# Performance work log

Hardware: AMD Instinct MI355X
Metric: run time of the kernel (lower is better)

Reference implementation:

```python
import jax, jax.numpy as jnp
import numpy as np

EPS = 1e-5

def conv1x1(x, w):
    # x: (B,C,H,W), w: (O,C) -> (B,O,H,W)
    return jnp.einsum('bchw,oc->bohw', x, w)

def bn_relu(y, g, b, m, v):
    s = g / jnp.sqrt(v + EPS)
    return jax.nn.relu(y * s[None, :, None, None] + (b - m * s)[None, :, None, None])

def cbr(x, w, g, b, m, v):
    return bn_relu(conv1x1(x, w), g, b, m, v)

def _bn_params(key, c):
    k1, k2, k3, k4 = jax.random.split(key, 4)
    g = 1.0 + 0.1 * jax.random.normal(k1, (c,), jnp.float32)
    b = 0.1 * jax.random.normal(k2, (c,), jnp.float32)
    m = 0.05 * jax.random.normal(k3, (c,), jnp.float32)
    v = jax.random.uniform(k4, (c,), jnp.float32, 0.5, 1.5)
    return g, b, m, v

def setup_inputs() -> dict:
    key = jax.random.key(0)
    B, Cin, H, W = 8, 512, 64, 64
    Ck, Cv, Cout = 256, 256, 512
    ks = jax.random.split(key, 12)
    def w(k, o, c):
        return jax.random.normal(k, (o, c), jnp.float32) * (1.0 / np.sqrt(c))
    inp = {}
    inp['x'] = jax.random.normal(ks[0], (B, Cin, H, W), jnp.float32)
    # f_key
    inp['kW1'] = w(ks[1], Ck, Cin); inp['kG1'], inp['kB1'], inp['kM1'], inp['kV1'] = _bn_params(ks[2], Ck)
    inp['kW2'] = w(ks[3], Ck, Ck);  inp['kG2'], inp['kB2'], inp['kM2'], inp['kV2'] = _bn_params(ks[4], Ck)
    # f_query
    inp['qW1'] = w(ks[5], Ck, Cin); inp['qG1'], inp['qB1'], inp['qM1'], inp['qV1'] = _bn_params(ks[6], Ck)
    inp['qW2'] = w(ks[7], Ck, Ck);  inp['qG2'], inp['qB2'], inp['qM2'], inp['qV2'] = _bn_params(ks[8], Ck)
    # f_value
    inp['vW'] = w(ks[9], Cv, Cin)
    # W (output projection)
    inp['wW'] = w(ks[10], Cout, Cv); inp['wG'], inp['wB'], inp['wM'], inp['wV'] = _bn_params(ks[11], Cout)
    return inp

def reference(x,
              kW1, kG1, kB1, kM1, kV1, kW2, kG2, kB2, kM2, kV2,
              qW1, qG1, qB1, qM1, qV1, qW2, qG2, qB2, qM2, qV2,
              vW,
              wW, wG, wB, wM, wV):
    B, _, H, W = x.shape
    q = cbr(cbr(x, qW1, qG1, qB1, qM1, qV1), qW2, qG2, qB2, qM2, qV2)  # (B,Ck,H,W)
    k = cbr(cbr(x, kW1, kG1, kB1, kM1, kV1), kW2, kG2, kB2, kM2, kV2)  # (B,Ck,H,W)
    v = conv1x1(x, vW)                                                  # (B,Cv,H,W)
    Ck = q.shape[1]; Cv = v.shape[1]; N = H * W
    qf = q.reshape(B, Ck, N)   # query = qf^T -> (B,N,Ck)
    kf = k.reshape(B, Ck, N)
    vf = v.reshape(B, Cv, N)
    sim = jnp.einsum('bcn,bcm->bnm', qf, kf) * (Ck ** -0.5)  # (B,N,N)
    attn = jax.nn.softmax(sim, axis=-1)
    ctx = jnp.einsum('bnm,bcm->bcn', attn, vf).reshape(B, Cv, H, W)
    return cbr(ctx, wW, wG, wB, wM, wV)
```

## Files before the change

### kernel.cpp

```cpp
#include <hip/hip_runtime.h>
#include <hip/hip_bf16.h>

typedef __attribute__((ext_vector_type(8))) short bf16x8;
typedef __attribute__((ext_vector_type(4))) float f32x4;

#define MFMA16(a, b, c) __builtin_amdgcn_mfma_f32_16x16x32_bf16(a, b, c, 0, 0, 0)

static __device__ __forceinline__ unsigned short f2bf(float f) {
  union { __hip_bfloat16 h; unsigned short u; } cv;
  cv.h = __float2bfloat16(f);
  return cv.u;
}

static __device__ __forceinline__ float bf2f(short s) {
  union { float f; unsigned u; } cv;
  cv.u = ((unsigned)(unsigned short)s) << 16;
  return cv.f;
}

static __device__ __forceinline__ void gload16(const void* gptr, void* lptr) {
  __builtin_amdgcn_global_load_lds(
      (const __attribute__((address_space(1))) void*)gptr,
      (__attribute__((address_space(3))) void*)lptr, 16, 0, 0);
}


__global__ void conv_w_k(const float* __restrict__ qW1, const float* __restrict__ kW1,
                         const float* __restrict__ qW2, const float* __restrict__ kW2,
                         const float* __restrict__ vW, const float* __restrict__ wW,
                         __hip_bfloat16* __restrict__ dst) {
  int i = blockIdx.x * 256 + threadIdx.x;
  const float* src; int off;
  if (i < 131072)      { src = qW1; off = i; }
  else if (i < 262144) { src = kW1; off = i - 131072; }
  else if (i < 327680) { src = qW2; off = i - 262144; }
  else if (i < 393216) { src = kW2; off = i - 327680; }
  else if (i < 524288) { src = vW;  off = i - 393216; }
  else                 { src = wW;  off = i - 524288; }
  dst[i] = __float2bfloat16(src[off]);
}

__global__ void bn_all_k(const float* __restrict__ qG1, const float* __restrict__ qB1, const float* __restrict__ qM1, const float* __restrict__ qV1,
                         const float* __restrict__ qG2, const float* __restrict__ qB2, const float* __restrict__ qM2, const float* __restrict__ qV2,
                         const float* __restrict__ kG1, const float* __restrict__ kB1, const float* __restrict__ kM1, const float* __restrict__ kV1,
                         const float* __restrict__ kG2, const float* __restrict__ kB2, const float* __restrict__ kM2, const float* __restrict__ kV2,
                         const float* __restrict__ wG, const float* __restrict__ wB, const float* __restrict__ wM, const float* __restrict__ wV,
                         float* __restrict__ base) {
  int bidx = blockIdx.x, tid = threadIdx.x;
  const float *g, *b, *m, *v; float *s, *t; int i;
  if (bidx == 0)      { g = qG1; b = qB1; m = qM1; v = qV1; s = base;        t = base + 256;  i = tid; }
  else if (bidx == 1) { g = qG2; b = qB2; m = qM2; v = qV2; s = base + 512;  t = base + 768;  i = tid; }
  else if (bidx == 2) { g = kG1; b = kB1; m = kM1; v = kV1; s = base + 1024; t = base + 1280; i = tid; }
  else if (bidx == 3) { g = kG2; b = kB2; m = kM2; v = kV2; s = base + 1536; t = base + 1792; i = tid; }
  else                { g = wG;  b = wB;  m = wM;  v = wV;  s = base + 2048; t = base + 2560; i = (bidx - 4) * 256 + tid; }
  float sv = g[i] * rsqrtf(v[i] + 1e-5f);
  s[i] = sv;
  t[i] = b[i] - m[i] * sv;
}

__global__ __launch_bounds__(256) void transpose_k(const float* __restrict__ x,
                                                   __hip_bfloat16* __restrict__ xT) {
  __shared__ float tile[64][65];
  const int n0 = blockIdx.x * 64, c0 = blockIdx.y * 64, b = blockIdx.z;
  const int tx = threadIdx.x, ty = threadIdx.y;
  const float* xp = x + ((size_t)(b * 512 + c0) * 4096) + n0;
#pragma unroll
  for (int i = 0; i < 16; ++i) {
    int c = ty + 4 * i;
    tile[c][tx] = xp[(size_t)c * 4096 + tx];
  }
  __syncthreads();
  __hip_bfloat16* op = xT + ((size_t)(b * 4096 + n0) * 512) + c0;
#pragma unroll
  for (int i = 0; i < 16; ++i) {
    int nl = ty + 4 * i;
    op[(size_t)nl * 512 + tx] = __float2bfloat16(tile[tx][nl]);
  }
}

template <int EPI>
__global__ __launch_bounds__(256) void gemm_nt_k(
    const __hip_bfloat16* __restrict__ A, long sA,
    const __hip_bfloat16* __restrict__ B, long sB,
    void* __restrict__ Cp, long sC,
    int lda, int ldb, int ldc, int K,
    const float* __restrict__ s, const float* __restrict__ t) {
  __shared__ short As[128][72];
  __shared__ short Bs[128][72];
  const int tid = threadIdx.x;
  const int w = tid >> 6, l = tid & 63, g = l >> 4, ln = l & 15;
  const int wr = w >> 1, wc = w & 1;
  const int rb = blockIdx.x * 128, cb = blockIdx.y * 128;
  const __hip_bfloat16* Ab = A + (size_t)blockIdx.z * sA;
  const __hip_bfloat16* Bb = B + (size_t)blockIdx.z * sB;

  f32x4 acc[4][4];
#pragma unroll
  for (int i = 0; i < 4; ++i)
#pragma unroll
    for (int j = 0; j < 4; ++j) acc[i][j] = (f32x4){0.f, 0.f, 0.f, 0.f};

  const int r0 = tid >> 3;
  const int c8 = (tid & 7) * 8;

  for (int k0 = 0; k0 < K; k0 += 64) {
#pragma unroll
    for (int i = 0; i < 4; ++i) {
      const int r = r0 + 32 * i;
      *(uint4*)&As[r][c8] = *(const uint4*)(Ab + (size_t)(rb + r) * lda + (k0 + c8));
      *(uint4*)&Bs[r][c8] = *(const uint4*)(Bb + (size_t)(cb + r) * ldb + (k0 + c8));
    }
    __syncthreads();
#pragma unroll
    for (int kk = 0; kk < 2; ++kk) {
      bf16x8 av[4], bv[4];
#pragma unroll
      for (int i = 0; i < 4; ++i) av[i] = *(const bf16x8*)&As[64 * wr + 16 * i + ln][32 * kk + 8 * g];
#pragma unroll
      for (int i = 0; i < 4; ++i) bv[i] = *(const bf16x8*)&Bs[64 * wc + 16 * i + ln][32 * kk + 8 * g];
#pragma unroll
      for (int mi = 0; mi < 4; ++mi)
#pragma unroll
        for (int ni = 0; ni < 4; ++ni)
          acc[mi][ni] = MFMA16(av[mi], bv[ni], acc[mi][ni]);
    }
    __syncthreads();
  }

  const int row0 = rb + 64 * wr + 4 * g;
  const int col0 = cb + 64 * wc + ln;

  if (EPI == 2) {
    float* C = (float*)Cp + (size_t)blockIdx.z * sC;
#pragma unroll
    for (int mi = 0; mi < 4; ++mi) {
#pragma unroll
      for (int r = 0; r < 4; ++r) {
        const int R = row0 + 16 * mi + r;
        const float sr = s[R], tr = t[R];
#pragma unroll
        for (int ni = 0; ni < 4; ++ni) {
          float v = fmaf(acc[mi][ni][r], sr, tr);
          C[(size_t)R * ldc + (col0 + 16 * ni)] = v > 0.f ? v : 0.f;
        }
      }
    }
  } else {
    __hip_bfloat16* C = (__hip_bfloat16*)Cp + (size_t)blockIdx.z * sC;
    float sc[4], tc[4];
    if (EPI == 1) {
#pragma unroll
      for (int ni = 0; ni < 4; ++ni) { sc[ni] = s[col0 + 16 * ni]; tc[ni] = t[col0 + 16 * ni]; }
    }
#pragma unroll
    for (int mi = 0; mi < 4; ++mi) {
#pragma unroll
      for (int ni = 0; ni < 4; ++ni) {
#pragma unroll
        for (int r = 0; r < 4; ++r) {
          float v = acc[mi][ni][r];
          if (EPI == 1) { v = fmaf(v, sc[ni], tc[ni]); v = v > 0.f ? v : 0.f; }
          C[(size_t)(row0 + 16 * mi + r) * ldc + (col0 + 16 * ni)] = __float2bfloat16(v);
        }
      }
    }
  }
}

__global__ __launch_bounds__(256, 2) void flash_k(
    const __hip_bfloat16* __restrict__ Q,
    const __hip_bfloat16* __restrict__ Kt,
    const __hip_bfloat16* __restrict__ V,
    __hip_bfloat16* __restrict__ part,
    float* __restrict__ cArr,
    float* __restrict__ lArr) {
  __shared__ short Ks[64 * 256];
  __shared__ short Ps[64 * 64];

  const int tid = threadIdx.x;
  const int w = tid >> 6, l = tid & 63, g = l >> 4, ln = l & 15;
  const int bid = blockIdx.x;
  const int batch = bid & 7;
  const int half = (bid >> 3) & 1;
  const int qb = (bid >> 4) << 6;
  const int kvBase = half << 11;
  const size_t bo = (size_t)batch * (4096 * 256);
  const float CE = 0.09016844005556021f;

  const int swz45 = (16 * g) ^ ((ln & 3) << 4);
  const int s6 = ((ln >> 2) & 1) << 6;
  const char* Ks0 = (const char*)Ks + (ln * 512 + swz45 + s6);
  const char* Ks1 = Ks0 + (((ln >> 2) & 1) ? -64 : 64);
  const char* Pr0 = (const char*)Ps + (ln * 128 + swz45 + s6);
  const char* Pr1 = Pr0 + (((ln >> 2) & 1) ? -64 : 64);
  const int pwOff = (16 * w + ln) * 128 + 8 * (g & 1) + (((g >> 1) ^ (ln & 1)) << 4) +
                    (((ln >> 1) & 1) << 5) + s6;

  bf16x8 qf[8];
  {
    const __hip_bfloat16* qp = Q + bo + (size_t)(qb + 16 * w + ln) * 256 + 8 * g;
#pragma unroll
    for (int kk = 0; kk < 8; ++kk) qf[kk] = *(const bf16x8*)(qp + 32 * kk);
  }

  f32x4 acc[4][4];
#pragma unroll
  for (int qg = 0; qg < 4; ++qg)
#pragma unroll
    for (int ci = 0; ci < 4; ++ci) acc[qg][ci] = (f32x4){0.f, 0.f, 0.f, 0.f};
  float l_run = 0.f;
  float cval = 0.f;

  const int kRow = 16 * w + (l >> 5);
  const int kChunk = (l & 31) ^ (l >> 5);
  const short* Kb = (const short*)(Kt + bo);
  const short* Vp = (const short*)(V + bo) + (size_t)(64 * w + ln) * 4096 + 8 * g;

#define SB __builtin_amdgcn_sched_barrier(0)

#define STAGEK(M0)                                                             \
  do {                                                                         \
    _Pragma("unroll") for (int j = 0; j < 8; ++j) {                            \
      const short* gp =                                                        \
          Kb + (size_t)((M0) + kRow + 2 * j) * 256 + 8 * (kChunk ^ ((2 * j) & 7)); \
      gload16(gp, Ks + w * 4096 + j * 512);                                    \
    }                                                                          \
  } while (0)

  STAGEK(kvBase);
  SB;

  for (int t = 0; t < 32; ++t) {
    const int m0 = kvBase + (t << 6);

    bf16x8 vfr[8];
#pragma unroll
    for (int ci = 0; ci < 4; ++ci)
#pragma unroll
      for (int kk = 0; kk < 2; ++kk) {
        const short* gp = Vp + (size_t)ci * (16 * 4096) + (m0 + 32 * kk);
        asm volatile("global_load_dwordx4 %0, %1, off"
                     : "=v"(vfr[2 * ci + kk]) : "v"(gp));
      }
    SB;

    asm volatile("s_waitcnt vmcnt(8)" ::: "memory");
    SB;
    __builtin_amdgcn_s_barrier();
    asm volatile("" ::: "memory");
    SB;

    f32x4 sf[4];
#pragma unroll
    for (int mi = 0; mi < 4; ++mi) sf[mi] = (f32x4){0.f, 0.f, 0.f, 0.f};
    __builtin_amdgcn_s_setprio(1);
#pragma unroll
    for (int kk = 0; kk < 8; ++kk) {
      const char* kp = ((kk & 1) ? Ks1 : Ks0) + 128 * (kk >> 1);
#pragma unroll
      for (int mi = 0; mi < 4; ++mi) {
        bf16x8 a = *(const bf16x8*)(kp + 8192 * mi);
        sf[mi] = MFMA16(a, qf[kk], sf[mi]);
      }
    }
    __builtin_amdgcn_s_setprio(0);

    if (t == 0) {
      float a0 = fmaxf(fmaxf(sf[0][0], sf[0][1]), sf[0][2]);
      float a1 = fmaxf(fmaxf(sf[0][3], sf[1][0]), sf[1][1]);
      float a2 = fmaxf(fmaxf(sf[1][2], sf[1][3]), sf[2][0]);
      float a3 = fmaxf(fmaxf(sf[2][1], sf[2][2]), sf[2][3]);
      float a4 = fmaxf(fmaxf(sf[3][0], sf[3][1]), sf[3][2]);
      float mmax = fmaxf(fmaxf(fmaxf(fmaxf(a0, a1), a2), fmaxf(a3, a4)), sf[3][3]);
      mmax = fmaxf(mmax, __shfl_xor(mmax, 16));
      mmax = fmaxf(mmax, __shfl_xor(mmax, 32));
      cval = mmax * CE;
    }
    float psum = 0.f;
    uint2 pk[4];
#pragma unroll
    for (int mi = 0; mi < 4; ++mi) {
      float e0 = exp2f(fmaf(sf[mi][0], CE, -cval));
      float e1 = exp2f(fmaf(sf[mi][1], CE, -cval));
      float e2 = exp2f(fmaf(sf[mi][2], CE, -cval));
      float e3 = exp2f(fmaf(sf[mi][3], CE, -cval));
      psum += (e0 + e1) + (e2 + e3);
      pk[mi].x = (unsigned)f2bf(e0) | ((unsigned)f2bf(e1) << 16);
      pk[mi].y = (unsigned)f2bf(e2) | ((unsigned)f2bf(e3) << 16);
    }
    psum += __shfl_xor(psum, 16);
    psum += __shfl_xor(psum, 32);
    l_run += psum;

    {
      char* Pb = (char*)Ps;
      *(uint2*)(Pb + (pwOff ^ 0))  = pk[0];
      *(uint2*)(Pb + (pwOff ^ 32)) = pk[1];
      *(uint2*)(Pb + (pwOff ^ 64)) = pk[2];
      *(uint2*)(Pb + (pwOff ^ 96)) = pk[3];
    }

    asm volatile("s_waitcnt lgkmcnt(0)" ::: "memory");
    SB;
    __builtin_amdgcn_s_barrier();
    asm volatile("" ::: "memory");
    SB;

    if (t < 31) {
      STAGEK(m0 + 64);
      SB;
      asm volatile("s_waitcnt vmcnt(8)" ::: "memory");
    } else {
      asm volatile("s_waitcnt vmcnt(0)" ::: "memory");
    }
    SB;

    __builtin_amdgcn_s_setprio(1);
#pragma unroll
    for (int kk = 0; kk < 2; ++kk) {
#pragma unroll
      for (int qg = 0; qg < 4; ++qg) {
        bf16x8 pa = *(const bf16x8*)((kk ? Pr1 : Pr0) + 2048 * qg);
#pragma unroll
        for (int ci = 0; ci < 4; ++ci)
          acc[qg][ci] = MFMA16(pa, vfr[2 * ci + kk], acc[qg][ci]);
      }
    }
    __builtin_amdgcn_s_setprio(0);
    SB;
  }
#undef STAGEK
#undef SB

  __syncthreads();
  float* Pf = (float*)Ps;
  if (g == 0) {
    Pf[16 * w + ln] = l_run;
    const int qi = (half * 8 + batch) * 4096 + qb + 16 * w + ln;
    cArr[qi] = cval;
    lArr[qi] = l_run;
  }
  __syncthreads();

  __hip_bfloat16* pb = part + ((size_t)(half * 8 + batch) * 4096 + qb) * 256;
#pragma unroll
  for (int qg = 0; qg < 4; ++qg) {
    f32x4 lv = *(const f32x4*)&Pf[16 * qg + 4 * g];
    f32x4 li;
#pragma unroll
    for (int r = 0; r < 4; ++r) li[r] = 1.0f / lv[r];
#pragma unroll
    for (int ci = 0; ci < 4; ++ci) {
#pragma unroll
      for (int r = 0; r < 4; ++r) {
        float val = acc[qg][ci][r] * li[r];
        pb[(size_t)(16 * qg + 4 * g + r) * 256 + 64 * w + 16 * ci + ln] = __float2bfloat16(val);
      }
    }
  }
}

__global__ __launch_bounds__(256) void merge_k(
    const __hip_bfloat16* __restrict__ part,
    const float* __restrict__ cArr, const float* __restrict__ lArr,
    __hip_bfloat16* __restrict__ ctx) {
  const int tid = threadIdx.x;
  const int R = blockIdx.x * 8 + (tid >> 5);
  const int cv = (tid & 31) * 8;
  const float c0 = cArr[R], c1 = cArr[32768 + R];
  const float l0 = lArr[R], l1 = lArr[32768 + R];
  const float Cm = fmaxf(c0, c1);
  float w0 = (l0 > 0.f) ? exp2f(c0 - Cm) * l0 : 0.f;
  float w1 = (l1 > 0.f) ? exp2f(c1 - Cm) * l1 : 0.f;
  const float sum = w0 + w1;
  const float inv = sum > 0.f ? 1.0f / sum : 0.f;
  w0 *= inv;
  w1 *= inv;
  const short* p0 = (const short*)part + (size_t)R * 256 + cv;
  const short* p1 = p0 + (size_t)32768 * 256;
  bf16x8 a0 = *(const bf16x8*)p0;
  bf16x8 a1 = *(const bf16x8*)p1;
  bf16x8 o;
#pragma unroll
  for (int j = 0; j < 8; ++j) {
    float v0 = (w0 > 0.f) ? w0 * bf2f(a0[j]) : 0.f;
    float v1 = (w1 > 0.f) ? w1 * bf2f(a1[j]) : 0.f;
    o[j] = (short)f2bf(v0 + v1);
  }
  *(bf16x8*)((short*)ctx + (size_t)R * 256 + cv) = o;
}


extern "C" void kernel_launch(void* const* d_in, const int* in_sizes, int n_in,
                              void* d_out, int out_size, void* d_ws, size_t ws_size,
                              hipStream_t stream) {
  const float* x   = (const float*)d_in[0];
  const float* kW1 = (const float*)d_in[1];
  const float* kG1 = (const float*)d_in[2];
  const float* kB1 = (const float*)d_in[3];
  const float* kM1 = (const float*)d_in[4];
  const float* kV1 = (const float*)d_in[5];
  const float* kW2 = (const float*)d_in[6];
  const float* kG2 = (const float*)d_in[7];
  const float* kB2 = (const float*)d_in[8];
  const float* kM2 = (const float*)d_in[9];
  const float* kV2 = (const float*)d_in[10];
  const float* qW1 = (const float*)d_in[11];
  const float* qG1 = (const float*)d_in[12];
  const float* qB1 = (const float*)d_in[13];
  const float* qM1 = (const float*)d_in[14];
  const float* qV1 = (const float*)d_in[15];
  const float* qW2 = (const float*)d_in[16];
  const float* qG2 = (const float*)d_in[17];
  const float* qB2 = (const float*)d_in[18];
  const float* qM2 = (const float*)d_in[19];
  const float* qV2 = (const float*)d_in[20];
  const float* vW  = (const float*)d_in[21];
  const float* wW  = (const float*)d_in[22];
  const float* wG  = (const float*)d_in[23];
  const float* wB  = (const float*)d_in[24];
  const float* wM  = (const float*)d_in[25];
  const float* wV  = (const float*)d_in[26];

  char* ws = (char*)d_ws;
  __hip_bfloat16* bQW1 = (__hip_bfloat16*)(ws + 0);
  __hip_bfloat16* bKW1 = (__hip_bfloat16*)(ws + 262144);
  __hip_bfloat16* bQW2 = (__hip_bfloat16*)(ws + 524288);
  __hip_bfloat16* bKW2 = (__hip_bfloat16*)(ws + 655360);
  __hip_bfloat16* bVW  = (__hip_bfloat16*)(ws + 786432);
  __hip_bfloat16* bWW  = (__hip_bfloat16*)(ws + 1048576);
  float* bnBase = (float*)(ws + 1310720);
  float* sQ1 = bnBase + 0;
  float* tQ1 = bnBase + 256;
  float* sQ2 = bnBase + 512;
  float* tQ2 = bnBase + 768;
  float* sK1 = bnBase + 1024;
  float* tK1 = bnBase + 1280;
  float* sK2 = bnBase + 1536;
  float* tK2 = bnBase + 1792;
  float* sWo = bnBase + 2048;
  float* tWo = bnBase + 2560;
  float* cArr = (float*)(ws + 1572864);
  float* lArr = (float*)(ws + 1835008);
  __hip_bfloat16* xT   = (__hip_bfloat16*)(ws + 2097152);
  __hip_bfloat16* bufA = (__hip_bfloat16*)(ws + 35651584);
  __hip_bfloat16* q2b  = (__hip_bfloat16*)(ws + 52428800);
  __hip_bfloat16* k2b  = (__hip_bfloat16*)(ws + 69206016);
  __hip_bfloat16* vB   = (__hip_bfloat16*)(ws + 85983232);

  conv_w_k<<<2560, 256, 0, stream>>>(qW1, kW1, qW2, kW2, vW, wW, bQW1);
  bn_all_k<<<6, 256, 0, stream>>>(qG1, qB1, qM1, qV1, qG2, qB2, qM2, qV2,
                                  kG1, kB1, kM1, kV1, kG2, kB2, kM2, kV2,
                                  wG, wB, wM, wV, bnBase);

  transpose_k<<<dim3(64, 8, 8), dim3(64, 4), 0, stream>>>(x, xT);

  gemm_nt_k<1><<<dim3(32, 2, 8), 256, 0, stream>>>(xT, 2097152L, bQW1, 0L, bufA, 1048576L,
                                                   512, 512, 256, 512, sQ1, tQ1);
  gemm_nt_k<1><<<dim3(32, 2, 8), 256, 0, stream>>>(bufA, 1048576L, bQW2, 0L, q2b, 1048576L,
                                                   256, 256, 256, 256, sQ2, tQ2);
  gemm_nt_k<1><<<dim3(32, 2, 8), 256, 0, stream>>>(xT, 2097152L, bKW1, 0L, bufA, 1048576L,
                                                   512, 512, 256, 512, sK1, tK1);
  gemm_nt_k<1><<<dim3(32, 2, 8), 256, 0, stream>>>(bufA, 1048576L, bKW2, 0L, k2b, 1048576L,
                                                   256, 256, 256, 256, sK2, tK2);
  gemm_nt_k<0><<<dim3(2, 32, 8), 256, 0, stream>>>(bVW, 0L, xT, 2097152L, vB, 1048576L,
                                                   512, 512, 4096, 512, nullptr, nullptr);
  flash_k<<<1024, 256, 0, stream>>>(q2b, k2b, vB, xT, cArr, lArr);
  merge_k<<<4096, 256, 0, stream>>>(xT, cArr, lArr, bufA);
  gemm_nt_k<2><<<dim3(4, 32, 8), 256, 0, stream>>>(bWW, 0L, bufA, 1048576L, d_out, 2097152L,
                                                   256, 256, 4096, 256, sWo, tWo);
}
```

Before: 308.2 us.

## Drop KV split in flash attention, use 128-key tiles, remove merge kernel

The flash attention kernel no longer splits the key range into two halves. Each block now covers all 4096 keys with 128-key tiles, which doubles the K shared-memory stage, P buffer and V register fragments. The separate merge kernel and its partial-output and statistics round trip through memory go away, and the kernel writes the normalized context directly. In exchange the grid halves to 512 blocks, which lowers parallelism on a large-CU GPU. The doubled LDS and register use may also cut occupancy, and exponents are now clamped to guard the fixed first-tile max against overflow.

```diff
diff --git a/kernel.cpp b/kernel.cpp
--- a/kernel.cpp
+++ b/kernel.cpp
@@ -10,12 +10,6 @@
   union { __hip_bfloat16 h; unsigned short u; } cv;
   cv.h = __float2bfloat16(f);
   return cv.u;
-}
-
-static __device__ __forceinline__ float bf2f(short s) {
-  union { float f; unsigned u; } cv;
-  cv.u = ((unsigned)(unsigned short)s) << 16;
-  return cv.f;
 }
 
 static __device__ __forceinline__ void gload16(const void* gptr, void* lptr) {
@@ -171,19 +165,15 @@
     const __hip_bfloat16* __restrict__ Q,
     const __hip_bfloat16* __restrict__ Kt,
     const __hip_bfloat16* __restrict__ V,
-    __hip_bfloat16* __restrict__ part,
-    float* __restrict__ cArr,
-    float* __restrict__ lArr) {
-  __shared__ short Ks[64 * 256];
-  __shared__ short Ps[64 * 64];
+    __hip_bfloat16* __restrict__ O) {
+  __shared__ short Ks[128 * 256];
+  __shared__ short Ps[64 * 128];
 
   const int tid = threadIdx.x;
   const int w = tid >> 6, l = tid & 63, g = l >> 4, ln = l & 15;
   const int bid = blockIdx.x;
   const int batch = bid & 7;
-  const int half = (bid >> 3) & 1;
-  const int qb = (bid >> 4) << 6;
-  const int kvBase = half << 11;
+  const int qb = (bid >> 3) << 6;
   const size_t bo = (size_t)batch * (4096 * 256);
   const float CE = 0.09016844005556021f;
 
@@ -191,9 +181,9 @@
   const int s6 = ((ln >> 2) & 1) << 6;
   const char* Ks0 = (const char*)Ks + (ln * 512 + swz45 + s6);
   const char* Ks1 = Ks0 + (((ln >> 2) & 1) ? -64 : 64);
-  const char* Pr0 = (const char*)Ps + (ln * 128 + swz45 + s6);
+  const char* Pr0 = (const char*)Ps + (ln * 256 + ((16 * g) ^ ((ln & 7) << 4)));
   const char* Pr1 = Pr0 + (((ln >> 2) & 1) ? -64 : 64);
-  const int pwOff = (16 * w + ln) * 128 + 8 * (g & 1) + (((g >> 1) ^ (ln & 1)) << 4) +
+  const int pwOff = (16 * w + ln) * 256 + 8 * (g & 1) + (((g >> 1) ^ (ln & 1)) << 4) +
                     (((ln >> 1) & 1) << 5) + s6;
 
   bf16x8 qf[8];
@@ -211,7 +201,7 @@
   float l_run = 0.f;
   float cval = 0.f;
 
-  const int kRow = 16 * w + (l >> 5);
+  const int kRow = 32 * w + (l >> 5);
   const int kChunk = (l & 31) ^ (l >> 5);
   const short* Kb = (const short*)(Kt + bo);
   const short* Vp = (const short*)(V + bo) + (size_t)(64 * w + ln) * 4096 + 8 * g;
@@ -220,45 +210,45 @@
 
 #define STAGEK(M0)                                                             \
   do {                                                                         \
-    _Pragma("unroll") for (int j = 0; j < 8; ++j) {                            \
+    _Pragma("unroll") for (int j = 0; j < 16; ++j) {                           \
       const short* gp =                                                        \
           Kb + (size_t)((M0) + kRow + 2 * j) * 256 + 8 * (kChunk ^ ((2 * j) & 7)); \
-      gload16(gp, Ks + w * 4096 + j * 512);                                    \
+      gload16(gp, Ks + w * 8192 + j * 512);                                    \
     }                                                                          \
   } while (0)
 
-  STAGEK(kvBase);
+  STAGEK(0);
   SB;
 
   for (int t = 0; t < 32; ++t) {
-    const int m0 = kvBase + (t << 6);
-
-    bf16x8 vfr[8];
+    const int m0 = t << 7;
+
+    bf16x8 vfr[16];
 #pragma unroll
     for (int ci = 0; ci < 4; ++ci)
 #pragma unroll
-      for (int kk = 0; kk < 2; ++kk) {
+      for (int kk = 0; kk < 4; ++kk) {
         const short* gp = Vp + (size_t)ci * (16 * 4096) + (m0 + 32 * kk);
         asm volatile("global_load_dwordx4 %0, %1, off"
-                     : "=v"(vfr[2 * ci + kk]) : "v"(gp));
-      }
-    SB;
-
-    asm volatile("s_waitcnt vmcnt(8)" ::: "memory");
+                     : "=v"(vfr[4 * ci + kk]) : "v"(gp));
+      }
+    SB;
+
+    asm volatile("s_waitcnt vmcnt(16)" ::: "memory");
     SB;
     __builtin_amdgcn_s_barrier();
     asm volatile("" ::: "memory");
     SB;
 
-    f32x4 sf[4];
-#pragma unroll
-    for (int mi = 0; mi < 4; ++mi) sf[mi] = (f32x4){0.f, 0.f, 0.f, 0.f};
+    f32x4 sf[8];
+#pragma unroll
+    for (int mi = 0; mi < 8; ++mi) sf[mi] = (f32x4){0.f, 0.f, 0.f, 0.f};
     __builtin_amdgcn_s_setprio(1);
 #pragma unroll
     for (int kk = 0; kk < 8; ++kk) {
       const char* kp = ((kk & 1) ? Ks1 : Ks0) + 128 * (kk >> 1);
 #pragma unroll
-      for (int mi = 0; mi < 4; ++mi) {
+      for (int mi = 0; mi < 8; ++mi) {
         bf16x8 a = *(const bf16x8*)(kp + 8192 * mi);
         sf[mi] = MFMA16(a, qf[kk], sf[mi]);
       }
@@ -266,24 +256,25 @@
     __builtin_amdgcn_s_setprio(0);
 
     if (t == 0) {
-      float a0 = fmaxf(fmaxf(sf[0][0], sf[0][1]), sf[0][2]);
-      float a1 = fmaxf(fmaxf(sf[0][3], sf[1][0]), sf[1][1]);
-      float a2 = fmaxf(fmaxf(sf[1][2], sf[1][3]), sf[2][0]);
-      float a3 = fmaxf(fmaxf(sf[2][1], sf[2][2]), sf[2][3]);
-      float a4 = fmaxf(fmaxf(sf[3][0], sf[3][1]), sf[3][2]);
-      float mmax = fmaxf(fmaxf(fmaxf(fmaxf(a0, a1), a2), fmaxf(a3, a4)), sf[3][3]);
+      float mmax = sf[0][0];
+#pragma unroll
+      for (int mi = 0; mi < 8; ++mi) {
+        float b0 = fmaxf(sf[mi][0], sf[mi][1]);
+        float b1 = fmaxf(sf[mi][2], sf[mi][3]);
+        mmax = fmaxf(mmax, fmaxf(b0, b1));
+      }
       mmax = fmaxf(mmax, __shfl_xor(mmax, 16));
       mmax = fmaxf(mmax, __shfl_xor(mmax, 32));
       cval = mmax * CE;
     }
     float psum = 0.f;
-    uint2 pk[4];
-#pragma unroll
-    for (int mi = 0; mi < 4; ++mi) {
-      float e0 = exp2f(fmaf(sf[mi][0], CE, -cval));
-      float e1 = exp2f(fmaf(sf[mi][1], CE, -cval));
-      float e2 = exp2f(fmaf(sf[mi][2], CE, -cval));
-      float e3 = exp2f(fmaf(sf[mi][3], CE, -cval));
+    uint2 pk[8];
+#pragma unroll
+    for (int mi = 0; mi < 8; ++mi) {
+      float e0 = exp2f(fminf(fmaf(sf[mi][0], CE, -cval), 40.0f));
+      float e1 = exp2f(fminf(fmaf(sf[mi][1], CE, -cval), 40.0f));
+      float e2 = exp2f(fminf(fmaf(sf[mi][2], CE, -cval), 40.0f));
+      float e3 = exp2f(fminf(fmaf(sf[mi][3], CE, -cval), 40.0f));
       psum += (e0 + e1) + (e2 + e3);
       pk[mi].x = (unsigned)f2bf(e0) | ((unsigned)f2bf(e1) << 16);
       pk[mi].y = (unsigned)f2bf(e2) | ((unsigned)f2bf(e3) << 16);
@@ -294,10 +285,9 @@
 
     {
       char* Pb = (char*)Ps;
-      *(uint2*)(Pb + (pwOff ^ 0))  = pk[0];
-      *(uint2*)(Pb + (pwOff ^ 32)) = pk[1];
-      *(uint2*)(Pb + (pwOff ^ 64)) = pk[2];
-      *(uint2*)(Pb + (pwOff ^ 96)) = pk[3];
+#pragma unroll
+      for (int mi = 0; mi < 8; ++mi)
+        *(uint2*)(Pb + ((pwOff ^ ((mi & 3) << 5)) + ((mi >> 2) << 7))) = pk[mi];
     }
 
     asm volatile("s_waitcnt lgkmcnt(0)" ::: "memory");
@@ -307,9 +297,9 @@
     SB;
 
     if (t < 31) {
-      STAGEK(m0 + 64);
+      STAGEK(m0 + 128);
       SB;
-      asm volatile("s_waitcnt vmcnt(8)" ::: "memory");
+      asm volatile("s_waitcnt vmcnt(16)" ::: "memory");
     } else {
       asm volatile("s_waitcnt vmcnt(0)" ::: "memory");
     }
@@ -317,13 +307,13 @@
 
     __builtin_amdgcn_s_setprio(1);
 #pragma unroll
-    for (int kk = 0; kk < 2; ++kk) {
+    for (int kk = 0; kk < 4; ++kk) {
 #pragma unroll
       for (int qg = 0; qg < 4; ++qg) {
-        bf16x8 pa = *(const bf16x8*)((kk ? Pr1 : Pr0) + 2048 * qg);
+        bf16x8 pa = *(const bf16x8*)(((kk & 1) ? Pr1 : Pr0) + 128 * (kk >> 1) + 4096 * qg);
 #pragma unroll
         for (int ci = 0; ci < 4; ++ci)
-          acc[qg][ci] = MFMA16(pa, vfr[2 * ci + kk], acc[qg][ci]);
+          acc[qg][ci] = MFMA16(pa, vfr[4 * ci + kk], acc[qg][ci]);
       }
     }
     __builtin_amdgcn_s_setprio(0);
@@ -334,15 +324,10 @@
 
   __syncthreads();
   float* Pf = (float*)Ps;
-  if (g == 0) {
-    Pf[16 * w + ln] = l_run;
-    const int qi = (half * 8 + batch) * 4096 + qb + 16 * w + ln;
-    cArr[qi] = cval;
-    lArr[qi] = l_run;
-  }
+  if (g == 0) Pf[16 * w + ln] = l_run;
   __syncthreads();
 
-  __hip_bfloat16* pb = part + ((size_t)(half * 8 + batch) * 4096 + qb) * 256;
+  __hip_bfloat16* Ob = O + bo;
 #pragma unroll
   for (int qg = 0; qg < 4; ++qg) {
     f32x4 lv = *(const f32x4*)&Pf[16 * qg + 4 * g];
@@ -354,40 +339,10 @@
 #pragma unroll
       for (int r = 0; r < 4; ++r) {
         float val = acc[qg][ci][r] * li[r];
-        pb[(size_t)(16 * qg + 4 * g + r) * 256 + 64 * w + 16 * ci + ln] = __float2bfloat16(val);
-      }
-    }
-  }
-}
-
-__global__ __launch_bounds__(256) void merge_k(
-    const __hip_bfloat16* __restrict__ part,
-    const float* __restrict__ cArr, const float* __restrict__ lArr,
-    __hip_bfloat16* __restrict__ ctx) {
-  const int tid = threadIdx.x;
-  const int R = blockIdx.x * 8 + (tid >> 5);
-  const int cv = (tid & 31) * 8;
-  const float c0 = cArr[R], c1 = cArr[32768 + R];
-  const float l0 = lArr[R], l1 = lArr[32768 + R];
-  const float Cm = fmaxf(c0, c1);
-  float w0 = (l0 > 0.f) ? exp2f(c0 - Cm) * l0 : 0.f;
-  float w1 = (l1 > 0.f) ? exp2f(c1 - Cm) * l1 : 0.f;
-  const float sum = w0 + w1;
-  const float inv = sum > 0.f ? 1.0f / sum : 0.f;
-  w0 *= inv;
-  w1 *= inv;
-  const short* p0 = (const short*)part + (size_t)R * 256 + cv;
-  const short* p1 = p0 + (size_t)32768 * 256;
-  bf16x8 a0 = *(const bf16x8*)p0;
-  bf16x8 a1 = *(const bf16x8*)p1;
-  bf16x8 o;
-#pragma unroll
-  for (int j = 0; j < 8; ++j) {
-    float v0 = (w0 > 0.f) ? w0 * bf2f(a0[j]) : 0.f;
-    float v1 = (w1 > 0.f) ? w1 * bf2f(a1[j]) : 0.f;
-    o[j] = (short)f2bf(v0 + v1);
-  }
-  *(bf16x8*)((short*)ctx + (size_t)R * 256 + cv) = o;
+        Ob[(size_t)(qb + 16 * qg + 4 * g + r) * 256 + 64 * w + 16 * ci + ln] = __float2bfloat16(val);
+      }
+    }
+  }
 }
 
 
@@ -440,8 +395,6 @@
   float* tK2 = bnBase + 1792;
   float* sWo = bnBase + 2048;
   float* tWo = bnBase + 2560;
-  float* cArr = (float*)(ws + 1572864);
-  float* lArr = (float*)(ws + 1835008);
   __hip_bfloat16* xT   = (__hip_bfloat16*)(ws + 2097152);
   __hip_bfloat16* bufA = (__hip_bfloat16*)(ws + 35651584);
   __hip_bfloat16* q2b  = (__hip_bfloat16*)(ws + 52428800);
@@ -465,8 +418,7 @@
                                                    256, 256, 256, 256, sK2, tK2);
   gemm_nt_k<0><<<dim3(2, 32, 8), 256, 0, stream>>>(bVW, 0L, xT, 2097152L, vB, 1048576L,
                                                    512, 512, 4096, 512, nullptr, nullptr);
-  flash_k<<<1024, 256, 0, stream>>>(q2b, k2b, vB, xT, cArr, lArr);
-  merge_k<<<4096, 256, 0, stream>>>(xT, cArr, lArr, bufA);
+  flash_k<<<512, 256, 0, stream>>>(q2b, k2b, vB, bufA);
   gemm_nt_k<2><<<dim3(4, 32, 8), 256, 0, stream>>>(bWW, 0L, bufA, 1048576L, d_out, 2097152L,
                                                    256, 256, 4096, 256, sWo, tWo);
 }
```

Measured after the change: 313.6 us. No clear change (+1.8%).
